# Kernel optimization log

Measured on AMD Instinct MI355X. Metric: run time of the kernel, lower is better.

Reference implementation:

```python
import jax, jax.numpy as jnp
import numpy as np

T, H, I, E, K = 1024, 2048, 1408, 8, 2  # tokens, hidden, moe_intermediate, n_experts, top_k

def setup_inputs() -> dict:
    key = jax.random.key(0)
    k0, k1, k2, k3 = jax.random.split(key, 4)
    def w(k, shape, fan_in):
        return jax.random.normal(k, shape, jnp.float32) / np.float32(np.sqrt(fan_in))
    return {
        "hidden_states": jax.random.normal(k0, (T, H), jnp.float32),
        "gate_w": w(k1, (H, E), H),      # router: LiteLinear(H -> E), no bias
        "w1": w(k2, (E, H, I), H),        # experts_w1 [E, H, I]
        "w2": w(k3, (E, I, H), I),        # experts_w2 [E, I, H]
    }

def reference(hidden_states, gate_w, w1, w2):
    # Router: logits -> softmax -> top-k expert probabilities (no renorm; Qwen2MoE norm_topk_prob=False)
    router_logits = hidden_states @ gate_w                      # [T, E]
    probs = jax.nn.softmax(router_logits, axis=-1)              # [T, E]
    topk_vals, topk_idx = jax.lax.top_k(probs, K)               # [T, K]
    # Dense combine weights: zero except at the top-k experts of each token
    combine = jnp.sum(jax.nn.one_hot(topk_idx, E, dtype=probs.dtype) * topk_vals[..., None], axis=1)  # [T, E]
    # Expert MLP per source: down(silu(x @ w1)) — note: no gate/up split in this repo's fused_moe weights
    h = jnp.einsum('th,ehi->tei', hidden_states, w1)            # [T, E, I]
    y = jnp.einsum('tei,eih->teh', jax.nn.silu(h), w2)          # [T, E, H]
    return jnp.einsum('te,teh->th', combine, y)                 # [T, H]
```

## Files before the change

### kernel.cpp

```cpp
#include <hip/hip_runtime.h>
#include <hip/hip_fp16.h>

#define T_TOK 1024
#define H_DIM 2048
#define I_DIM 1408
#define N_EXP 8
#define TOPK  2

using f16x8 = __attribute__((ext_vector_type(8))) _Float16;
using f32x4 = __attribute__((ext_vector_type(4))) float;

#define BM 128
#define BN 64
#define BK 64
#define NTHR 512

#define BAR()                                                     \
    do {                                                          \
        asm volatile("s_waitcnt lgkmcnt(0)" ::: "memory");        \
        __builtin_amdgcn_s_barrier();                             \
    } while (0)

#define WS_COUNTS      0
#define WS_BASES       256
#define WS_CURSORS     512
#define WS_TOPK_E      768
#define WS_TOPK_W      (768 + 8192)
#define WS_TOK_OF_SLOT 17408
#define WS_W_OF_SLOT   29696
#define WS_HACT        43008
#define WS_NEEDED      (43008 + 8650752)

__global__ void k_router(const float* __restrict__ X, const float* __restrict__ GW,
                         int* __restrict__ counts, int* __restrict__ topk_e,
                         float* __restrict__ topk_w) {
    int t = (blockIdx.x * blockDim.x + threadIdx.x) >> 6;
    int lane = threadIdx.x & 63;
    if (t >= T_TOK) return;
    float acc[N_EXP];
#pragma unroll
    for (int e = 0; e < N_EXP; ++e) acc[e] = 0.f;
    const float* xrow = X + (size_t)t * H_DIM;
    for (int h = lane; h < H_DIM; h += 64) {
        float x = xrow[h];
        const float* g = GW + (size_t)h * N_EXP;
#pragma unroll
        for (int e = 0; e < N_EXP; ++e) acc[e] = fmaf(x, g[e], acc[e]);
    }
#pragma unroll
    for (int off = 32; off > 0; off >>= 1) {
#pragma unroll
        for (int e = 0; e < N_EXP; ++e) acc[e] += __shfl_xor(acc[e], off, 64);
    }
    if (lane == 0) {
        float m = acc[0];
#pragma unroll
        for (int e = 1; e < N_EXP; ++e) m = fmaxf(m, acc[e]);
        float ex[N_EXP], s = 0.f;
#pragma unroll
        for (int e = 0; e < N_EXP; ++e) { ex[e] = expf(acc[e] - m); s += ex[e]; }
        float inv = 1.f / s;
        int e1 = 0;
#pragma unroll
        for (int e = 1; e < N_EXP; ++e) if (ex[e] > ex[e1]) e1 = e;
        int e2 = (e1 == 0) ? 1 : 0;
#pragma unroll
        for (int e = 0; e < N_EXP; ++e) if (e != e1 && ex[e] > ex[e2]) e2 = e;
        topk_e[t * 2 + 0] = e1;
        topk_e[t * 2 + 1] = e2;
        topk_w[t * 2 + 0] = ex[e1] * inv;
        topk_w[t * 2 + 1] = ex[e2] * inv;
        atomicAdd(&counts[e1], 1);
        atomicAdd(&counts[e2], 1);
    }
}

__global__ void k_prefix(const int* __restrict__ counts, int* __restrict__ bases,
                         int* __restrict__ cursors) {
    if (threadIdx.x == 0) {
        int b = 0;
        for (int e = 0; e < N_EXP; ++e) {
            bases[e] = b;
            b += ((counts[e] + BM - 1) / BM) * BM;
            cursors[e] = 0;
        }
    }
}

__global__ void k_scatter(const int* __restrict__ topk_e, const float* __restrict__ topk_w,
                          const int* __restrict__ bases, int* __restrict__ cursors,
                          int* __restrict__ tok_of_slot, float* __restrict__ w_of_slot) {
    int t = blockIdx.x * blockDim.x + threadIdx.x;
    if (t >= T_TOK) return;
    for (int j = 0; j < TOPK; ++j) {
        int e = topk_e[t * 2 + j];
        int pos = atomicAdd(&cursors[e], 1);
        int slot = bases[e] + pos;
        tok_of_slot[slot] = t;
        w_of_slot[slot] = topk_w[t * 2 + j];
    }
}


#define G_COMPUTE(buf)                                                          \
    do {                                                                        \
        _Pragma("unroll") for (int ks = 0; ks < 2; ++ks) {                      \
            f16x8 af[2], bf[2];                                                 \
            _Pragma("unroll") for (int ii = 0; ii < 2; ++ii) {                  \
                int r = wm + ii * 16 + rsel;                                    \
                af[ii] = *(const f16x8*)&As[buf][r][((kq + 4 * ks) ^ (r & 7)) * 8]; \
            }                                                                   \
            _Pragma("unroll") for (int jj = 0; jj < 2; ++jj) {                  \
                int r = wn + jj * 16 + rsel;                                    \
                bf[jj] = *(const f16x8*)&Bs[buf][r][((kq + 4 * ks) ^ (r & 7)) * 8]; \
            }                                                                   \
            _Pragma("unroll") for (int ii = 0; ii < 2; ++ii)                    \
                _Pragma("unroll") for (int jj = 0; jj < 2; ++jj)                \
                    acc[ii][jj] = __builtin_amdgcn_mfma_f32_16x16x32_f16(af[ii], bf[jj], acc[ii][jj], 0, 0, 0); \
        }                                                                       \
    } while (0)

__global__ __launch_bounds__(NTHR, 4) void k_gemm1(
    const float* __restrict__ X, const float* __restrict__ W1,
    const int* __restrict__ counts, const int* __restrict__ bases,
    const int* __restrict__ tok_of_slot, const float* __restrict__ w_of_slot,
    _Float16* __restrict__ hact) {
    __shared__ _Float16 As[2][BM][BK];
    __shared__ _Float16 Bs[2][BN][BK];

    const int e = blockIdx.z;
    const int cnt = counts[e];
    const int m0 = blockIdx.y * BM;
    if (m0 >= cnt) return;
    const int base = bases[e];
    const int n0 = blockIdx.x * BN;
    const int tid = threadIdx.x;

    const int ar = tid >> 2;
    const int ac2 = (tid & 3) * 2;
    const int r_eff = min(ar, cnt - m0 - 1);
    const float* arow = X + (size_t)tok_of_slot[base + m0 + r_eff] * H_DIM + (tid & 3) * 16;

    const int bn = tid & 63;
    const int bc = tid >> 6;
    const float* bcol = W1 + (size_t)e * (H_DIM * I_DIM) + (size_t)(bc * 8) * I_DIM + n0 + bn;

    const int wid = tid >> 6, lane = tid & 63;
    const int wm = (wid >> 1) * 32, wn = (wid & 1) * 32;
    const int rsel = lane & 15, kq = lane >> 4;

    f32x4 acc[2][2] = {};

    float4 aR0[4]; float bR0[8];
    float4 aR1[4]; float bR1[8];

#define LOAD1(aR, bR, k0)                                              \
    do {                                                               \
        aR[0] = *(const float4*)(arow + (k0));                         \
        aR[1] = *(const float4*)(arow + (k0) + 4);                     \
        aR[2] = *(const float4*)(arow + (k0) + 8);                     \
        aR[3] = *(const float4*)(arow + (k0) + 12);                    \
        const float* bp = bcol + (size_t)(k0) * I_DIM;                 \
        _Pragma("unroll") for (int j = 0; j < 8; ++j)                  \
            bR[j] = bp[(size_t)j * I_DIM];                             \
    } while (0)

#define STORE1(buf, aR, bR)                                            \
    do {                                                               \
        f16x8 p0, p1;                                                  \
        _Pragma("unroll") for (int j = 0; j < 4; ++j) {                \
            p0[j]     = (_Float16)aR[0][j];                            \
            p0[j + 4] = (_Float16)aR[1][j];                            \
            p1[j]     = (_Float16)aR[2][j];                            \
            p1[j + 4] = (_Float16)aR[3][j];                            \
        }                                                              \
        *(f16x8*)&As[buf][ar][((ac2) ^ (ar & 7)) * 8] = p0;            \
        *(f16x8*)&As[buf][ar][((ac2 + 1) ^ (ar & 7)) * 8] = p1;        \
        f16x8 q;                                                       \
        _Pragma("unroll") for (int j = 0; j < 8; ++j)                  \
            q[j] = (_Float16)bR[j];                                    \
        *(f16x8*)&Bs[buf][bn][(bc ^ (bn & 7)) * 8] = q;                \
    } while (0)

    const int KT = H_DIM / BK;
    LOAD1(aR0, bR0, 0);
    STORE1(0, aR0, bR0);
    LOAD1(aR0, bR0, BK);
    BAR();
    for (int kt = 0; kt < KT; kt += 2) {
        if (kt + 2 < KT) LOAD1(aR1, bR1, (kt + 2) * BK);
        G_COMPUTE(0);
        if (kt + 1 < KT) STORE1(1, aR0, bR0);
        BAR();
        if (kt + 3 < KT) LOAD1(aR0, bR0, (kt + 3) * BK);
        if (kt + 1 < KT) {
            G_COMPUTE(1);
            if (kt + 2 < KT) STORE1(0, aR1, bR1);
            BAR();
        }
    }
#undef LOAD1
#undef STORE1

    const int rows = cnt - m0;
#pragma unroll
    for (int i = 0; i < 2; ++i) {
#pragma unroll
        for (int rg = 0; rg < 4; ++rg) {
            int r = wm + i * 16 + kq * 4 + rg;
            if (r < rows) {
                int slot = base + m0 + r;
                float w = w_of_slot[slot];
                _Float16* hrow = hact + (size_t)slot * I_DIM + n0;
#pragma unroll
                for (int j = 0; j < 2; ++j) {
                    float v = acc[i][j][rg];
                    hrow[wn + j * 16 + rsel] = (_Float16)(v / (1.f + expf(-v)) * w);
                }
            }
        }
    }
}

__global__ __launch_bounds__(NTHR, 4) void k_gemm2(
    const _Float16* __restrict__ hact, const float* __restrict__ W2,
    const int* __restrict__ counts, const int* __restrict__ bases,
    const int* __restrict__ tok_of_slot, float* __restrict__ out) {
    __shared__ _Float16 As[2][BM][BK];
    __shared__ _Float16 Bs[2][BN][BK];

    const int e = blockIdx.z;
    const int cnt = counts[e];
    const int m0 = blockIdx.y * BM;
    if (m0 >= cnt) return;
    const int base = bases[e];
    const int n0 = blockIdx.x * BN;
    const int tid = threadIdx.x;

    const int ar = tid >> 2;
    const int ac2 = (tid & 3) * 2;
    const int r_eff = min(ar, cnt - m0 - 1);
    const _Float16* arow = hact + (size_t)(base + m0 + r_eff) * I_DIM + (tid & 3) * 16;

    const int bn = tid & 63;
    const int bc = tid >> 6;
    const float* bcol = W2 + (size_t)e * (I_DIM * H_DIM) + (size_t)(bc * 8) * H_DIM + n0 + bn;

    const int wid = tid >> 6, lane = tid & 63;
    const int wm = (wid >> 1) * 32, wn = (wid & 1) * 32;
    const int rsel = lane & 15, kq = lane >> 4;

    f32x4 acc[2][2] = {};

    f16x8 aR0[2]; float bR0[8];
    f16x8 aR1[2]; float bR1[8];

#define LOAD2(aR, bR, k0)                                              \
    do {                                                               \
        aR[0] = *(const f16x8*)(arow + (k0));                          \
        aR[1] = *(const f16x8*)(arow + (k0) + 8);                      \
        const float* bp = bcol + (size_t)(k0) * H_DIM;                 \
        _Pragma("unroll") for (int j = 0; j < 8; ++j)                  \
            bR[j] = bp[(size_t)j * H_DIM];                             \
    } while (0)

#define STORE2(buf, aR, bR)                                            \
    do {                                                               \
        *(f16x8*)&As[buf][ar][((ac2) ^ (ar & 7)) * 8] = aR[0];         \
        *(f16x8*)&As[buf][ar][((ac2 + 1) ^ (ar & 7)) * 8] = aR[1];     \
        f16x8 q;                                                       \
        _Pragma("unroll") for (int j = 0; j < 8; ++j)                  \
            q[j] = (_Float16)bR[j];                                    \
        *(f16x8*)&Bs[buf][bn][(bc ^ (bn & 7)) * 8] = q;                \
    } while (0)

    const int KT = I_DIM / BK;
    LOAD2(aR0, bR0, 0);
    STORE2(0, aR0, bR0);
    LOAD2(aR0, bR0, BK);
    BAR();
    for (int kt = 0; kt < KT; kt += 2) {
        if (kt + 2 < KT) LOAD2(aR1, bR1, (kt + 2) * BK);
        G_COMPUTE(0);
        if (kt + 1 < KT) STORE2(1, aR0, bR0);
        BAR();
        if (kt + 3 < KT) LOAD2(aR0, bR0, (kt + 3) * BK);
        if (kt + 1 < KT) {
            G_COMPUTE(1);
            if (kt + 2 < KT) STORE2(0, aR1, bR1);
            BAR();
        }
    }
#undef LOAD2
#undef STORE2

    const int rows = cnt - m0;
#pragma unroll
    for (int i = 0; i < 2; ++i) {
#pragma unroll
        for (int rg = 0; rg < 4; ++rg) {
            int r = wm + i * 16 + kq * 4 + rg;
            if (r < rows) {
                int slot = base + m0 + r;
                int tok = tok_of_slot[slot];
                float* orow = out + (size_t)tok * H_DIM + n0;
#pragma unroll
                for (int j = 0; j < 2; ++j)
                    atomicAdd(&orow[wn + j * 16 + rsel], acc[i][j][rg]);
            }
        }
    }
}

extern "C" void kernel_launch(void* const* d_in, const int* in_sizes, int n_in,
                              void* d_out, int out_size, void* d_ws, size_t ws_size,
                              hipStream_t stream) {
    const float* X  = (const float*)d_in[0];
    const float* GW = (const float*)d_in[1];
    const float* W1 = (const float*)d_in[2];
    const float* W2 = (const float*)d_in[3];
    float* out = (float*)d_out;
    char* ws = (char*)d_ws;
    if (ws_size < (size_t)WS_NEEDED) return;

    int*   counts      = (int*)(ws + WS_COUNTS);
    int*   bases       = (int*)(ws + WS_BASES);
    int*   cursors     = (int*)(ws + WS_CURSORS);
    int*   topk_e      = (int*)(ws + WS_TOPK_E);
    float* topk_w      = (float*)(ws + WS_TOPK_W);
    int*   tok_of_slot = (int*)(ws + WS_TOK_OF_SLOT);
    float* w_of_slot   = (float*)(ws + WS_W_OF_SLOT);
    _Float16* hact     = (_Float16*)(ws + WS_HACT);

    hipMemsetAsync(counts, 0, N_EXP * sizeof(int), stream);
    hipMemsetAsync(out, 0, (size_t)T_TOK * H_DIM * sizeof(float), stream);
    k_router<<<T_TOK / 4, 256, 0, stream>>>(X, GW, counts, topk_e, topk_w);
    k_prefix<<<1, 64, 0, stream>>>(counts, bases, cursors);
    k_scatter<<<T_TOK / 256, 256, 0, stream>>>(topk_e, topk_w, bases, cursors,
                                               tok_of_slot, w_of_slot);
    k_gemm1<<<dim3(I_DIM / BN, T_TOK / BM, N_EXP), NTHR, 0, stream>>>(
        X, W1, counts, bases, tok_of_slot, w_of_slot, hact);
    k_gemm2<<<dim3(H_DIM / BN, T_TOK / BM, N_EXP), NTHR, 0, stream>>>(
        hact, W2, counts, bases, tok_of_slot, out);
}
```

Measured before the change: 167.8 us.

## Drop prefix kernel and memsets, halve M tile, read A operands directly from global

Removes the k_prefix launch by recomputing expert bases inline from counts, folds output zeroing into the router kernel, and merges the two memsets into one workspace memset. The GEMMs move to BM=64 with 256 threads, load the A operand straight from global memory into MFMA registers instead of staging it in LDS, and stage 16 B values per thread. This cuts launch overhead and LDS traffic and gives more blocks for expert imbalance. The cost is uncoalesced, unbuffered per-lane A loads and fp32-to-fp16 conversion of A on every tile, and W1/W2 are now read for twice as many M tiles.

```diff
diff --git a/kernel.cpp b/kernel.cpp
--- a/kernel.cpp
+++ b/kernel.cpp
@@ -10,10 +10,10 @@
 using f16x8 = __attribute__((ext_vector_type(8))) _Float16;
 using f32x4 = __attribute__((ext_vector_type(4))) float;
 
-#define BM 128
+#define BM 64
 #define BN 64
 #define BK 64
-#define NTHR 512
+#define NTHR 256
 
 #define BAR()                                                     \
     do {                                                          \
@@ -22,7 +22,6 @@
     } while (0)
 
 #define WS_COUNTS      0
-#define WS_BASES       256
 #define WS_CURSORS     512
 #define WS_TOPK_E      768
 #define WS_TOPK_W      (768 + 8192)
@@ -31,10 +30,25 @@
 #define WS_HACT        43008
 #define WS_NEEDED      (43008 + 8650752)
 
+__device__ __forceinline__ void prefix_of(const int* counts, int e, int& base, int& cnt) {
+    int b = 0;
+#pragma unroll
+    for (int q = 0; q < N_EXP; ++q) {
+        int c = counts[q];
+        if (q == e) { base = b; cnt = c; }
+        b += ((c + BM - 1) / BM) * BM;
+    }
+}
+
 __global__ void k_router(const float* __restrict__ X, const float* __restrict__ GW,
                          int* __restrict__ counts, int* __restrict__ topk_e,
-                         float* __restrict__ topk_w) {
-    int t = (blockIdx.x * blockDim.x + threadIdx.x) >> 6;
+                         float* __restrict__ topk_w, float* __restrict__ out) {
+    int gtid = blockIdx.x * blockDim.x + threadIdx.x;
+    float4* o4 = (float4*)out;
+    for (int i = gtid; i < T_TOK * H_DIM / 4; i += (T_TOK / 4) * 256)
+        o4[i] = float4{0.f, 0.f, 0.f, 0.f};
+
+    int t = gtid >> 6;
     int lane = threadIdx.x & 63;
     if (t >= T_TOK) return;
     float acc[N_EXP];
@@ -75,132 +89,120 @@
     }
 }
 
-__global__ void k_prefix(const int* __restrict__ counts, int* __restrict__ bases,
-                         int* __restrict__ cursors) {
-    if (threadIdx.x == 0) {
-        int b = 0;
-        for (int e = 0; e < N_EXP; ++e) {
-            bases[e] = b;
-            b += ((counts[e] + BM - 1) / BM) * BM;
-            cursors[e] = 0;
-        }
-    }
-}
-
 __global__ void k_scatter(const int* __restrict__ topk_e, const float* __restrict__ topk_w,
-                          const int* __restrict__ bases, int* __restrict__ cursors,
+                          const int* __restrict__ counts, int* __restrict__ cursors,
                           int* __restrict__ tok_of_slot, float* __restrict__ w_of_slot) {
     int t = blockIdx.x * blockDim.x + threadIdx.x;
     if (t >= T_TOK) return;
     for (int j = 0; j < TOPK; ++j) {
         int e = topk_e[t * 2 + j];
+        int base, cnt;
+        prefix_of(counts, e, base, cnt);
         int pos = atomicAdd(&cursors[e], 1);
-        int slot = bases[e] + pos;
+        int slot = base + pos;
         tok_of_slot[slot] = t;
         w_of_slot[slot] = topk_w[t * 2 + j];
     }
 }
 
 
-#define G_COMPUTE(buf)                                                          \
+#define MFMA4()                                                                 \
+    _Pragma("unroll") for (int ii = 0; ii < 2; ++ii)                            \
+        _Pragma("unroll") for (int jj = 0; jj < 2; ++jj)                        \
+            acc[ii][jj] = __builtin_amdgcn_mfma_f32_16x16x32_f16(af[ii], bf[jj], acc[ii][jj], 0, 0, 0);
+
+#define BF_READ(buf, ks)                                                        \
+    _Pragma("unroll") for (int jj = 0; jj < 2; ++jj) {                          \
+        int col = wn + jj * 16 + rsel;                                          \
+        bf[jj] = *(const f16x8*)&Bs[buf][col][((kq + 4 * (ks)) ^ (col & 7)) * 8]; \
+    }
+
+#define LOADB(bS, k0)                                                           \
+    do {                                                                        \
+        const float* bp = bcol + (size_t)(k0) * LDB;                            \
+        _Pragma("unroll") for (int j = 0; j < 16; ++j)                          \
+            bS[j] = bp[(size_t)j * LDB];                                        \
+    } while (0)
+
+#define STOREB(buf, bS)                                                         \
+    do {                                                                        \
+        f16x8 q0, q1;                                                           \
+        _Pragma("unroll") for (int j = 0; j < 8; ++j) {                         \
+            q0[j] = (_Float16)bS[j]; q1[j] = (_Float16)bS[j + 8];               \
+        }                                                                       \
+        *(f16x8*)&Bs[buf][bn][((bc2) ^ (bn & 7)) * 8] = q0;                     \
+        *(f16x8*)&Bs[buf][bn][((bc2 + 1) ^ (bn & 7)) * 8] = q1;                 \
+    } while (0)
+
+__global__ __launch_bounds__(NTHR, 4) void k_gemm1(
+    const float* __restrict__ X, const float* __restrict__ W1,
+    const int* __restrict__ counts, const int* __restrict__ tok_of_slot,
+    const float* __restrict__ w_of_slot, _Float16* __restrict__ hact) {
+    __shared__ _Float16 Bs[2][BN][BK];
+
+    const int e = blockIdx.z;
+    int base, cnt;
+    prefix_of(counts, e, base, cnt);
+    const int m0 = blockIdx.y * BM;
+    if (m0 >= cnt) return;
+    const int n0 = blockIdx.x * BN;
+    const int tid = threadIdx.x;
+    const int LDB = I_DIM;
+
+    const int bn = tid & 63;
+    const int bc2 = (tid >> 6) * 2;
+    const float* bcol = W1 + (size_t)e * (H_DIM * I_DIM) + (size_t)(bc2 * 8) * I_DIM + n0 + bn;
+
+    const int wid = tid >> 6, lane = tid & 63;
+    const int wm = (wid >> 1) * 32, wn = (wid & 1) * 32;
+    const int rsel = lane & 15, kq = lane >> 4;
+
+    const float* arowp[2];
+#pragma unroll
+    for (int ii = 0; ii < 2; ++ii) {
+        int r = wm + ii * 16 + rsel;
+        int rr = min(r, cnt - m0 - 1);
+        arowp[ii] = X + (size_t)tok_of_slot[base + m0 + rr] * H_DIM + kq * 8;
+    }
+
+    f32x4 acc[2][2] = {};
+    float bS0[16], bS1[16];
+
+#define COMPUTE1(buf, kbase)                                                    \
     do {                                                                        \
         _Pragma("unroll") for (int ks = 0; ks < 2; ++ks) {                      \
             f16x8 af[2], bf[2];                                                 \
             _Pragma("unroll") for (int ii = 0; ii < 2; ++ii) {                  \
-                int r = wm + ii * 16 + rsel;                                    \
-                af[ii] = *(const f16x8*)&As[buf][r][((kq + 4 * ks) ^ (r & 7)) * 8]; \
+                float a8[8];                                                    \
+                const float* ap = arowp[ii] + (kbase) + ks * 32;                \
+                *(float4*)(a8 + 0) = *(const float4*)(ap);                      \
+                *(float4*)(a8 + 4) = *(const float4*)(ap + 4);                  \
+                _Pragma("unroll") for (int c = 0; c < 8; ++c)                   \
+                    af[ii][c] = (_Float16)a8[c];                                \
             }                                                                   \
-            _Pragma("unroll") for (int jj = 0; jj < 2; ++jj) {                  \
-                int r = wn + jj * 16 + rsel;                                    \
-                bf[jj] = *(const f16x8*)&Bs[buf][r][((kq + 4 * ks) ^ (r & 7)) * 8]; \
-            }                                                                   \
-            _Pragma("unroll") for (int ii = 0; ii < 2; ++ii)                    \
-                _Pragma("unroll") for (int jj = 0; jj < 2; ++jj)                \
-                    acc[ii][jj] = __builtin_amdgcn_mfma_f32_16x16x32_f16(af[ii], bf[jj], acc[ii][jj], 0, 0, 0); \
+            BF_READ(buf, ks);                                                   \
+            MFMA4();                                                            \
         }                                                                       \
     } while (0)
 
-__global__ __launch_bounds__(NTHR, 4) void k_gemm1(
-    const float* __restrict__ X, const float* __restrict__ W1,
-    const int* __restrict__ counts, const int* __restrict__ bases,
-    const int* __restrict__ tok_of_slot, const float* __restrict__ w_of_slot,
-    _Float16* __restrict__ hact) {
-    __shared__ _Float16 As[2][BM][BK];
-    __shared__ _Float16 Bs[2][BN][BK];
-
-    const int e = blockIdx.z;
-    const int cnt = counts[e];
-    const int m0 = blockIdx.y * BM;
-    if (m0 >= cnt) return;
-    const int base = bases[e];
-    const int n0 = blockIdx.x * BN;
-    const int tid = threadIdx.x;
-
-    const int ar = tid >> 2;
-    const int ac2 = (tid & 3) * 2;
-    const int r_eff = min(ar, cnt - m0 - 1);
-    const float* arow = X + (size_t)tok_of_slot[base + m0 + r_eff] * H_DIM + (tid & 3) * 16;
-
-    const int bn = tid & 63;
-    const int bc = tid >> 6;
-    const float* bcol = W1 + (size_t)e * (H_DIM * I_DIM) + (size_t)(bc * 8) * I_DIM + n0 + bn;
-
-    const int wid = tid >> 6, lane = tid & 63;
-    const int wm = (wid >> 1) * 32, wn = (wid & 1) * 32;
-    const int rsel = lane & 15, kq = lane >> 4;
-
-    f32x4 acc[2][2] = {};
-
-    float4 aR0[4]; float bR0[8];
-    float4 aR1[4]; float bR1[8];
-
-#define LOAD1(aR, bR, k0)                                              \
-    do {                                                               \
-        aR[0] = *(const float4*)(arow + (k0));                         \
-        aR[1] = *(const float4*)(arow + (k0) + 4);                     \
-        aR[2] = *(const float4*)(arow + (k0) + 8);                     \
-        aR[3] = *(const float4*)(arow + (k0) + 12);                    \
-        const float* bp = bcol + (size_t)(k0) * I_DIM;                 \
-        _Pragma("unroll") for (int j = 0; j < 8; ++j)                  \
-            bR[j] = bp[(size_t)j * I_DIM];                             \
-    } while (0)
-
-#define STORE1(buf, aR, bR)                                            \
-    do {                                                               \
-        f16x8 p0, p1;                                                  \
-        _Pragma("unroll") for (int j = 0; j < 4; ++j) {                \
-            p0[j]     = (_Float16)aR[0][j];                            \
-            p0[j + 4] = (_Float16)aR[1][j];                            \
-            p1[j]     = (_Float16)aR[2][j];                            \
-            p1[j + 4] = (_Float16)aR[3][j];                            \
-        }                                                              \
-        *(f16x8*)&As[buf][ar][((ac2) ^ (ar & 7)) * 8] = p0;            \
-        *(f16x8*)&As[buf][ar][((ac2 + 1) ^ (ar & 7)) * 8] = p1;        \
-        f16x8 q;                                                       \
-        _Pragma("unroll") for (int j = 0; j < 8; ++j)                  \
-            q[j] = (_Float16)bR[j];                                    \
-        *(f16x8*)&Bs[buf][bn][(bc ^ (bn & 7)) * 8] = q;                \
-    } while (0)
-
-    const int KT = H_DIM / BK;
-    LOAD1(aR0, bR0, 0);
-    STORE1(0, aR0, bR0);
-    LOAD1(aR0, bR0, BK);
+    constexpr int KT = H_DIM / BK;
+    LOADB(bS0, 0);
+    STOREB(0, bS0);
+    LOADB(bS0, BK);
     BAR();
     for (int kt = 0; kt < KT; kt += 2) {
-        if (kt + 2 < KT) LOAD1(aR1, bR1, (kt + 2) * BK);
-        G_COMPUTE(0);
-        if (kt + 1 < KT) STORE1(1, aR0, bR0);
+        if (kt + 2 < KT) LOADB(bS1, (kt + 2) * BK);
+        COMPUTE1(0, kt * BK);
+        if (kt + 1 < KT) STOREB(1, bS0);
         BAR();
-        if (kt + 3 < KT) LOAD1(aR0, bR0, (kt + 3) * BK);
+        if (kt + 3 < KT) LOADB(bS0, (kt + 3) * BK);
         if (kt + 1 < KT) {
-            G_COMPUTE(1);
-            if (kt + 2 < KT) STORE1(0, aR1, bR1);
+            COMPUTE1(1, (kt + 1) * BK);
+            if (kt + 2 < KT) STOREB(0, bS1);
             BAR();
         }
     }
-#undef LOAD1
-#undef STORE1
+#undef COMPUTE1
 
     const int rows = cnt - m0;
 #pragma unroll
@@ -224,75 +226,67 @@
 
 __global__ __launch_bounds__(NTHR, 4) void k_gemm2(
     const _Float16* __restrict__ hact, const float* __restrict__ W2,
-    const int* __restrict__ counts, const int* __restrict__ bases,
-    const int* __restrict__ tok_of_slot, float* __restrict__ out) {
-    __shared__ _Float16 As[2][BM][BK];
+    const int* __restrict__ counts, const int* __restrict__ tok_of_slot,
+    float* __restrict__ out) {
     __shared__ _Float16 Bs[2][BN][BK];
 
     const int e = blockIdx.z;
-    const int cnt = counts[e];
+    int base, cnt;
+    prefix_of(counts, e, base, cnt);
     const int m0 = blockIdx.y * BM;
     if (m0 >= cnt) return;
-    const int base = bases[e];
     const int n0 = blockIdx.x * BN;
     const int tid = threadIdx.x;
-
-    const int ar = tid >> 2;
-    const int ac2 = (tid & 3) * 2;
-    const int r_eff = min(ar, cnt - m0 - 1);
-    const _Float16* arow = hact + (size_t)(base + m0 + r_eff) * I_DIM + (tid & 3) * 16;
+    const int LDB = H_DIM;
 
     const int bn = tid & 63;
-    const int bc = tid >> 6;
-    const float* bcol = W2 + (size_t)e * (I_DIM * H_DIM) + (size_t)(bc * 8) * H_DIM + n0 + bn;
+    const int bc2 = (tid >> 6) * 2;
+    const float* bcol = W2 + (size_t)e * (I_DIM * H_DIM) + (size_t)(bc2 * 8) * H_DIM + n0 + bn;
 
     const int wid = tid >> 6, lane = tid & 63;
     const int wm = (wid >> 1) * 32, wn = (wid & 1) * 32;
     const int rsel = lane & 15, kq = lane >> 4;
 
+    const _Float16* arowp[2];
+#pragma unroll
+    for (int ii = 0; ii < 2; ++ii) {
+        int r = wm + ii * 16 + rsel;
+        int rr = min(r, cnt - m0 - 1);
+        arowp[ii] = hact + (size_t)(base + m0 + rr) * I_DIM + kq * 8;
+    }
+
     f32x4 acc[2][2] = {};
-
-    f16x8 aR0[2]; float bR0[8];
-    f16x8 aR1[2]; float bR1[8];
-
-#define LOAD2(aR, bR, k0)                                              \
-    do {                                                               \
-        aR[0] = *(const f16x8*)(arow + (k0));                          \
-        aR[1] = *(const f16x8*)(arow + (k0) + 8);                      \
-        const float* bp = bcol + (size_t)(k0) * H_DIM;                 \
-        _Pragma("unroll") for (int j = 0; j < 8; ++j)                  \
-            bR[j] = bp[(size_t)j * H_DIM];                             \
-    } while (0)
-
-#define STORE2(buf, aR, bR)                                            \
-    do {                                                               \
-        *(f16x8*)&As[buf][ar][((ac2) ^ (ar & 7)) * 8] = aR[0];         \
-        *(f16x8*)&As[buf][ar][((ac2 + 1) ^ (ar & 7)) * 8] = aR[1];     \
-        f16x8 q;                                                       \
-        _Pragma("unroll") for (int j = 0; j < 8; ++j)                  \
-            q[j] = (_Float16)bR[j];                                    \
-        *(f16x8*)&Bs[buf][bn][(bc ^ (bn & 7)) * 8] = q;                \
-    } while (0)
-
-    const int KT = I_DIM / BK;
-    LOAD2(aR0, bR0, 0);
-    STORE2(0, aR0, bR0);
-    LOAD2(aR0, bR0, BK);
+    float bS0[16], bS1[16];
+
+#define COMPUTE2(buf, kbase)                                                    \
+    do {                                                                        \
+        _Pragma("unroll") for (int ks = 0; ks < 2; ++ks) {                      \
+            f16x8 af[2], bf[2];                                                 \
+            _Pragma("unroll") for (int ii = 0; ii < 2; ++ii)                    \
+                af[ii] = *(const f16x8*)(arowp[ii] + (kbase) + ks * 32);        \
+            BF_READ(buf, ks);                                                   \
+            MFMA4();                                                            \
+        }                                                                       \
+    } while (0)
+
+    constexpr int KT = I_DIM / BK;
+    LOADB(bS0, 0);
+    STOREB(0, bS0);
+    LOADB(bS0, BK);
     BAR();
     for (int kt = 0; kt < KT; kt += 2) {
-        if (kt + 2 < KT) LOAD2(aR1, bR1, (kt + 2) * BK);
-        G_COMPUTE(0);
-        if (kt + 1 < KT) STORE2(1, aR0, bR0);
+        if (kt + 2 < KT) LOADB(bS1, (kt + 2) * BK);
+        COMPUTE2(0, kt * BK);
+        if (kt + 1 < KT) STOREB(1, bS0);
         BAR();
-        if (kt + 3 < KT) LOAD2(aR0, bR0, (kt + 3) * BK);
+        if (kt + 3 < KT) LOADB(bS0, (kt + 3) * BK);
         if (kt + 1 < KT) {
-            G_COMPUTE(1);
-            if (kt + 2 < KT) STORE2(0, aR1, bR1);
+            COMPUTE2(1, (kt + 1) * BK);
+            if (kt + 2 < KT) STOREB(0, bS1);
             BAR();
         }
     }
-#undef LOAD2
-#undef STORE2
+#undef COMPUTE2
 
     const int rows = cnt - m0;
 #pragma unroll
@@ -324,7 +318,6 @@
     if (ws_size < (size_t)WS_NEEDED) return;
 
     int*   counts      = (int*)(ws + WS_COUNTS);
-    int*   bases       = (int*)(ws + WS_BASES);
     int*   cursors     = (int*)(ws + WS_CURSORS);
     int*   topk_e      = (int*)(ws + WS_TOPK_E);
     float* topk_w      = (float*)(ws + WS_TOPK_W);
@@ -332,14 +325,12 @@
     float* w_of_slot   = (float*)(ws + WS_W_OF_SLOT);
     _Float16* hact     = (_Float16*)(ws + WS_HACT);
 
-    hipMemsetAsync(counts, 0, N_EXP * sizeof(int), stream);
-    hipMemsetAsync(out, 0, (size_t)T_TOK * H_DIM * sizeof(float), stream);
-    k_router<<<T_TOK / 4, 256, 0, stream>>>(X, GW, counts, topk_e, topk_w);
-    k_prefix<<<1, 64, 0, stream>>>(counts, bases, cursors);
-    k_scatter<<<T_TOK / 256, 256, 0, stream>>>(topk_e, topk_w, bases, cursors,
+    hipMemsetAsync(ws, 0, 768, stream);
+    k_router<<<T_TOK / 4, 256, 0, stream>>>(X, GW, counts, topk_e, topk_w, out);
+    k_scatter<<<T_TOK / 256, 256, 0, stream>>>(topk_e, topk_w, counts, cursors,
                                                tok_of_slot, w_of_slot);
-    k_gemm1<<<dim3(I_DIM / BN, T_TOK / BM, N_EXP), NTHR, 0, stream>>>(
-        X, W1, counts, bases, tok_of_slot, w_of_slot, hact);
-    k_gemm2<<<dim3(H_DIM / BN, T_TOK / BM, N_EXP), NTHR, 0, stream>>>(
-        hact, W2, counts, bases, tok_of_slot, out);
-}
+    k_gemm1<<<dim3(I_DIM / BN, 16, N_EXP), NTHR, 0, stream>>>(
+        X, W1, counts, tok_of_slot, w_of_slot, hact);
+    k_gemm2<<<dim3(H_DIM / BN, 16, N_EXP), NTHR, 0, stream>>>(
+        hact, W2, counts, tok_of_slot, out);
+}
```

Result: slower. 269.3 us (+60.5%).
